# Kernel optimization log

Hardware: AMD Instinct MI355X
Metric: run time of the kernel (lower is better)

Reference implementation:

```python
import jax, jax.numpy as jnp
import numpy as np

N_NODES = 100000
N_EDGES = 500000
HIDDEN = 256


def setup_inputs() -> dict:
    key = jax.random.key(0)
    k_x, k_e, k_w1, k_b1, k_w2, k_b2 = jax.random.split(key, 6)
    x = jax.random.normal(k_x, (N_NODES, HIDDEN), dtype=jnp.float32)
    edge_label_index = jax.random.randint(k_e, (2, N_EDGES), 0, N_NODES, dtype=jnp.int64)
    # fc1: Linear(2*hidden -> hidden); fc2: Linear(hidden -> 1). PyTorch stores W as [out, in].
    bound1 = 1.0 / np.sqrt(2 * HIDDEN)
    W1 = jax.random.uniform(k_w1, (HIDDEN, 2 * HIDDEN), dtype=jnp.float32, minval=-bound1, maxval=bound1)
    b1 = jax.random.uniform(k_b1, (HIDDEN,), dtype=jnp.float32, minval=-bound1, maxval=bound1)
    bound2 = 1.0 / np.sqrt(HIDDEN)
    W2 = jax.random.uniform(k_w2, (1, HIDDEN), dtype=jnp.float32, minval=-bound2, maxval=bound2)
    b2 = jax.random.uniform(k_b2, (1,), dtype=jnp.float32, minval=-bound2, maxval=bound2)
    return {"x": x, "edge_label_index": edge_label_index, "W1": W1, "b1": b1, "W2": W2, "b2": b2}


def reference(x, edge_label_index, W1, b1, W2, b2):
    # Gather endpoint features: [E, H] each
    feat_src = x[edge_label_index[0]]
    feat_dst = x[edge_label_index[1]]
    h = jnp.concatenate([feat_src, feat_dst], axis=1)  # [E, 2H]
    h = jax.nn.relu(h @ W1.T + b1)                      # [E, H]
    out = jax.nn.sigmoid(h @ W2.T + b2)                 # [E, 1]
    return out.reshape(-1)
```

## Files before the change

### kernel.cpp

```cpp
#include <hip/hip_runtime.h>
#include <math.h>

#define NNODES 100000
#define MT     64
#define NTILES 1563
#define NODESP (NTILES * MT)
#define NEDGES 500000
#define HID    256
#define K2     512
#define GEMM_GRID 256

typedef _Float16 h8v __attribute__((ext_vector_type(8)));
typedef _Float16 h2v __attribute__((ext_vector_type(2)));
typedef __fp16   fp16x2 __attribute__((ext_vector_type(2)));
typedef __bf16   bf16x8 __attribute__((ext_vector_type(8)));
typedef float    f32x4  __attribute__((ext_vector_type(4)));

__device__ __forceinline__ unsigned short f2bf(float f) {
    unsigned int u = __float_as_uint(f);
    u += 0x7FFFu + ((u >> 16) & 1u);
    return (unsigned short)(u >> 16);
}
__device__ __forceinline__ void async16(void* lds, const void* g) {
    __builtin_amdgcn_global_load_lds((const __attribute__((address_space(1))) void*)g,
                                     (__attribute__((address_space(3))) void*)lds, 16, 0, 0);
}

__global__ void cvt_w1h(const float* __restrict__ W1, _Float16* __restrict__ Bsw) {
    int t = blockIdx.x * 256 + threadIdx.x;
    if (t >= 8 * 32 * 64) return;
    int lane = t & 63, nt = (t >> 6) & 31, kt = t >> 11;
    int j = nt * 16 + (lane & 15);
    int k = kt * 32 + ((lane >> 4) << 3);
    const float* src = W1 + (size_t)(j & 255) * K2 + ((j >> 8) << 8) + k;
    union { _Float16 s[8]; uint4 v; } u;
#pragma unroll
    for (int jj = 0; jj < 8; ++jj) u.s[jj] = (_Float16)src[jj];
    ((uint4*)Bsw)[t] = u.v;
}

__global__ void cvt_w2p(const float* __restrict__ W2, float* __restrict__ w2p) {
    int t = threadIdx.x;
    int i = (t >> 2) & 15, nt = t & 3;
    w2p[t] = W2[(t & ~63) | (nt * 16 + i)];
}

__global__ __launch_bounds__(512, 2) void node_gemm6(
    const float* __restrict__ x,
    const _Float16* __restrict__ Bsw,
    const float* __restrict__ b1,
    _Float16* __restrict__ UV)
{
    __shared__ __align__(16) float Afs[2][64 * 256];
    const int tid  = threadIdx.x;
    const int lane = tid & 63;
    const int wave = tid >> 6;

    const h8v* B8 = (const h8v*)Bsw;
    h8v barr[8][4];
#pragma unroll
    for (int ks = 0; ks < 8; ++ks)
#pragma unroll
        for (int nt = 0; nt < 4; ++nt)
            barr[ks][nt] = B8[((size_t)(ks * 32 + wave * 4 + nt)) * 64 + lane];

    float b1v[4];
#pragma unroll
    for (int nt = 0; nt < 4; ++nt) {
        int col = wave * 64 + nt * 16 + (lane & 15);
        b1v[nt] = (col < 256) ? b1[col] : 0.0f;
    }

    const int rlo = lane & 15;
    const int chi = (lane >> 4) << 1;

    auto issue = [&](int tile, int buf) {
        uint4* A4 = (uint4*)Afs[buf];
#pragma unroll
        for (int i = 0; i < 8; ++i) {
            int idx  = wave * 8 + i;
            int ks   = idx >> 3;
            int mt   = (idx >> 1) & 3;
            int half = idx & 1;
            int row  = tile * MT + mt * 16 + rlo;
            int rl   = row < NNODES ? row : 0;
            int c    = ks * 8 + chi + half;
            async16(&A4[idx * 64], x + (size_t)rl * 256 + c * 4);
        }
    };

    int tile = blockIdx.x;
    issue(tile, 0);
    __syncthreads();
    int buf = 0;

    while (true) {
        int next = tile + GEMM_GRID;
        bool has_next = next < NTILES;
        if (has_next) issue(next, buf ^ 1);

        f32x4 acc[4][4] = {};
        const float4* AF = (const float4*)Afs[buf];
#pragma unroll
        for (int ks = 0; ks < 8; ++ks) {
#pragma unroll
            for (int mt = 0; mt < 4; ++mt) {
                int idx = (ks * 4 + mt) * 2;
                float4 r0 = AF[idx * 64 + lane];
                float4 r1 = AF[(idx + 1) * 64 + lane];
                union { fp16x2 p[4]; h8v v; } af;
                af.p[0] = __builtin_amdgcn_cvt_pkrtz(r0.x, r0.y);
                af.p[1] = __builtin_amdgcn_cvt_pkrtz(r0.z, r0.w);
                af.p[2] = __builtin_amdgcn_cvt_pkrtz(r1.x, r1.y);
                af.p[3] = __builtin_amdgcn_cvt_pkrtz(r1.z, r1.w);
#pragma unroll
                for (int nt = 0; nt < 4; ++nt)
                    acc[mt][nt] = __builtin_amdgcn_mfma_f32_16x16x32_f16(
                        af.v, barr[ks][nt], acc[mt][nt], 0, 0, 0);
            }
        }

#pragma unroll
        for (int mt = 0; mt < 4; ++mt) {
#pragma unroll
            for (int r = 0; r < 4; ++r) {
                int row = tile * MT + mt * 16 + ((lane >> 4) << 2) + r;
                union { _Float16 h[4]; uint2 v; } pk;
#pragma unroll
                for (int nt = 0; nt < 4; ++nt)
                    pk.h[nt] = (_Float16)(acc[mt][nt][r] + b1v[nt]);
                *(uint2*)(UV + (size_t)row * 512 + wave * 64 + (lane & 15) * 4) = pk.v;
            }
        }

        if (!has_next) break;
        __syncthreads();
        buf ^= 1;
        tile = next;
    }
}

__global__ __launch_bounds__(256) void edge_out5(
    const _Float16* __restrict__ UV,
    const int* __restrict__ ei,
    const float* __restrict__ w2p,
    const float* __restrict__ b2,
    float* __restrict__ out)
{
    const int tid = threadIdx.x;
    const int q   = tid & 31;
    const int g   = tid >> 5;
    const long e  = ((long)blockIdx.x * 8 + g) * 8;
    if (e >= NEDGES) return;

    int4 s0 = *(const int4*)(ei + e);
    int4 s1 = *(const int4*)(ei + e + 4);
    int4 d0 = *(const int4*)(ei + NEDGES + e);
    int4 d1 = *(const int4*)(ei + NEDGES + e + 4);
    int is[8] = {s0.x, s0.y, s0.z, s0.w, s1.x, s1.y, s1.z, s1.w};
    int id[8] = {d0.x, d0.y, d0.z, d0.w, d1.x, d1.y, d1.z, d1.w};

    union U8 { uint4 v; h2v h[4]; };
    const _Float16* up = UV + q * 8;

    U8 uu[8], vv[8];
#pragma unroll
    for (int ed = 0; ed < 8; ++ed) {
        uu[ed].v = *(const uint4*)(up + (size_t)is[ed] * 512);
        vv[ed].v = *(const uint4*)(up + (size_t)id[ed] * 512 + 256);
    }

    h2v w2h[4];
    {
        const float4* pw = (const float4*)w2p + q * 2;
        float4 c = pw[0], d = pw[1];
        w2h[0] = h2v{(_Float16)c.x, (_Float16)c.y};
        w2h[1] = h2v{(_Float16)c.z, (_Float16)c.w};
        w2h[2] = h2v{(_Float16)d.x, (_Float16)d.y};
        w2h[3] = h2v{(_Float16)d.z, (_Float16)d.w};
    }

    const h2v zz = {(_Float16)0.0f, (_Float16)0.0f};
    float z[8];
#pragma unroll
    for (int ed = 0; ed < 8; ++ed) {
        float zt = 0.f;
#pragma unroll
        for (int p = 0; p < 4; ++p) {
            h2v h = uu[ed].h[p] + vv[ed].h[p];
            h = __builtin_elementwise_max(h, zz);
            zt = __builtin_amdgcn_fdot2(h, w2h[p], zt, false);
        }
        z[ed] = zt;
    }
#pragma unroll
    for (int m = 1; m < 32; m <<= 1) {
#pragma unroll
        for (int ed = 0; ed < 8; ++ed)
            z[ed] += __shfl_xor(z[ed], m, 32);
    }
    if (q < 8) {
        float zq = (q == 0) ? z[0] : (q == 1) ? z[1] : (q == 2) ? z[2] :
                   (q == 3) ? z[3] : (q == 4) ? z[4] : (q == 5) ? z[5] :
                   (q == 6) ? z[6] : z[7];
        out[e + q] = 1.0f / (1.0f + expf(-(zq + b2[0])));
    }
}

__global__ void cvt_w1_r1(const float* __restrict__ W1, unsigned short* __restrict__ Bsw) {
    int t = blockIdx.x * 256 + threadIdx.x;
    if (t >= 16 * 16 * 64) return;
    int lane = t & 63, nt = (t >> 6) & 15, kt = t >> 10;
    int n = nt * 16 + (lane & 15);
    int k = kt * 32 + ((lane >> 4) << 3);
    const float* src = W1 + (size_t)n * K2 + k;
    union { unsigned short s[8]; uint4 v; } u;
#pragma unroll
    for (int j = 0; j < 8; ++j) u.s[j] = f2bf(src[j]);
    ((uint4*)Bsw)[t] = u.v;
}

__global__ __launch_bounds__(256) void edge_mlp_fb(
    const float* __restrict__ xf, const int* __restrict__ ei,
    const unsigned short* __restrict__ Bsw, const float* __restrict__ b1,
    const float* __restrict__ W2, const float* __restrict__ b2,
    float* __restrict__ out)
{
    __shared__ __align__(16) unsigned short Asw[8 * 4 * 64 * 8];
    __shared__ float es[64];
    const int tid = threadIdx.x, lane = tid & 63, wave = tid >> 6;
    const int e0 = blockIdx.x * 64;
    if (tid < 64) es[tid] = 0.0f;
    f32x4 acc[4][4] = {};
    const bf16x8* A8 = (const bf16x8*)Asw;
    const bf16x8* B8 = (const bf16x8*)Bsw;
    for (int h = 0; h < 2; ++h) {
#pragma unroll
        for (int i = 0; i < 8; ++i) {
            int m = i * 8 + wave * 2 + (lane >> 5);
            int e = e0 + m;
            int ee = (e < NEDGES) ? e : 0;
            int node = ei[(size_t)h * NEDGES + ee];
            int chunk = lane & 31;
            const float4* p = (const float4*)(xf + ((size_t)node << 8) + (chunk << 3));
            float4 a = p[0], bq = p[1];
            union { unsigned short s[8]; uint4 v4; } u;
            u.s[0] = f2bf(a.x);  u.s[1] = f2bf(a.y);  u.s[2] = f2bf(a.z);  u.s[3] = f2bf(a.w);
            u.s[4] = f2bf(bq.x); u.s[5] = f2bf(bq.y); u.s[6] = f2bf(bq.z); u.s[7] = f2bf(bq.w);
            int ktl = chunk >> 2, qq = chunk & 3;
            int u16 = ((ktl * 4 + (m >> 4)) << 6) + (qq << 4) + (m & 15);
            u16 ^= (u16 >> 8) & 7;
            ((uint4*)Asw)[u16] = u.v4;
        }
        __syncthreads();
#pragma unroll
        for (int kt = 0; kt < 8; ++kt) {
            bf16x8 af[4], bfr[4];
#pragma unroll
            for (int mt = 0; mt < 4; ++mt) {
                int u16 = ((kt * 4 + mt) << 6) + lane;
                u16 ^= (u16 >> 8) & 7;
                af[mt] = A8[u16];
            }
#pragma unroll
            for (int nt = 0; nt < 4; ++nt)
                bfr[nt] = B8[(((h * 8 + kt) << 4) + (wave << 2) + nt) * 64 + lane];
#pragma unroll
            for (int mt = 0; mt < 4; ++mt)
#pragma unroll
                for (int nt = 0; nt < 4; ++nt)
                    acc[mt][nt] = __builtin_amdgcn_mfma_f32_16x16x32_bf16(
                        af[mt], bfr[nt], acc[mt][nt], 0, 0, 0);
        }
        __syncthreads();
    }
    float w2v[4], b1v[4];
#pragma unroll
    for (int nt = 0; nt < 4; ++nt) {
        int n = (wave << 6) + (nt << 4) + (lane & 15);
        w2v[nt] = W2[n]; b1v[nt] = b1[n];
    }
#pragma unroll
    for (int mt = 0; mt < 4; ++mt) {
#pragma unroll
        for (int r = 0; r < 4; ++r) {
            float p = 0.0f;
#pragma unroll
            for (int nt = 0; nt < 4; ++nt) {
                float hv = acc[mt][nt][r] + b1v[nt];
                p = fmaf(fmaxf(hv, 0.0f), w2v[nt], p);
            }
            p += __shfl_xor(p, 1, 16);
            p += __shfl_xor(p, 2, 16);
            p += __shfl_xor(p, 4, 16);
            p += __shfl_xor(p, 8, 16);
            if ((lane & 15) == 0)
                atomicAdd(&es[(mt << 4) + ((lane >> 4) << 2) + r], p);
        }
    }
    __syncthreads();
    if (tid < 64) {
        int e = e0 + tid;
        if (e < NEDGES) out[e] = 1.0f / (1.0f + expf(-(es[tid] + b2[0])));
    }
}

extern "C" void kernel_launch(void* const* d_in, const int* in_sizes, int n_in,
                              void* d_out, int out_size, void* d_ws, size_t ws_size,
                              hipStream_t stream) {
    const float* x  = (const float*)d_in[0];
    const int*   ei = (const int*)d_in[1];
    const float* W1 = (const float*)d_in[2];
    const float* b1 = (const float*)d_in[3];
    const float* W2 = (const float*)d_in[4];
    const float* b2 = (const float*)d_in[5];
    float* out = (float*)d_out;

    const size_t BSW_BYTES = 1 << 18;
    const size_t W2P_BYTES = 4096;
    const size_t UV_BYTES  = (size_t)NODESP * K2 * 2;
    const size_t NEED_A = BSW_BYTES + W2P_BYTES + UV_BYTES;

    if (ws_size >= NEED_A) {
        _Float16* Bsw = (_Float16*)d_ws;
        float*    w2p = (float*)((char*)d_ws + BSW_BYTES);
        _Float16* UV  = (_Float16*)((char*)d_ws + BSW_BYTES + W2P_BYTES);
        cvt_w1h<<<64, 256, 0, stream>>>(W1, Bsw);
        cvt_w2p<<<1, 256, 0, stream>>>(W2, w2p);
        node_gemm6<<<GEMM_GRID, 512, 0, stream>>>(x, Bsw, b1, UV);
        edge_out5<<<7813, 256, 0, stream>>>(UV, ei, w2p, b2, out);
    } else {
        unsigned short* Bsw = (unsigned short*)d_ws;
        cvt_w1_r1<<<64, 256, 0, stream>>>(W1, Bsw);
        edge_mlp_fb<<<(NEDGES + 63) / 64, 256, 0, stream>>>(x, ei, Bsw, b1, W2, b2, out);
    }
}
```

Before: 256.8 us.

## Load GEMM A operand directly from global into registers, dropping LDS staging

The node GEMM no longer stages x tiles in shared memory through async global-to-LDS copies with double buffering and barriers. Each wave now reads its own rows straight from global memory into registers, prefetching one MFMA step ahead. This removes the 128KB LDS footprint and the block-wide barriers, but every wave reloads the same A rows, so L2 traffic rises eightfold and the register-level prefetch hides less latency than the deeper LDS pipeline did.

```diff
diff --git a/kernel.cpp b/kernel.cpp
--- a/kernel.cpp
+++ b/kernel.cpp
@@ -21,10 +21,6 @@
     u += 0x7FFFu + ((u >> 16) & 1u);
     return (unsigned short)(u >> 16);
 }
-__device__ __forceinline__ void async16(void* lds, const void* g) {
-    __builtin_amdgcn_global_load_lds((const __attribute__((address_space(1))) void*)g,
-                                     (__attribute__((address_space(3))) void*)lds, 16, 0, 0);
-}
 
 __global__ void cvt_w1h(const float* __restrict__ W1, _Float16* __restrict__ Bsw) {
     int t = blockIdx.x * 256 + threadIdx.x;
@@ -45,13 +41,12 @@
     w2p[t] = W2[(t & ~63) | (nt * 16 + i)];
 }
 
-__global__ __launch_bounds__(512, 2) void node_gemm6(
+__global__ __launch_bounds__(512, 2) void node_gemm7(
     const float* __restrict__ x,
     const _Float16* __restrict__ Bsw,
     const float* __restrict__ b1,
     _Float16* __restrict__ UV)
 {
-    __shared__ __align__(16) float Afs[2][64 * 256];
     const int tid  = threadIdx.x;
     const int lane = tid & 63;
     const int wave = tid >> 6;
@@ -71,53 +66,42 @@
         b1v[nt] = (col < 256) ? b1[col] : 0.0f;
     }
 
-    const int rlo = lane & 15;
-    const int chi = (lane >> 4) << 1;
-
-    auto issue = [&](int tile, int buf) {
-        uint4* A4 = (uint4*)Afs[buf];
-#pragma unroll
-        for (int i = 0; i < 8; ++i) {
-            int idx  = wave * 8 + i;
-            int ks   = idx >> 3;
-            int mt   = (idx >> 1) & 3;
-            int half = idx & 1;
-            int row  = tile * MT + mt * 16 + rlo;
-            int rl   = row < NNODES ? row : 0;
-            int c    = ks * 8 + chi + half;
-            async16(&A4[idx * 64], x + (size_t)rl * 256 + c * 4);
-        }
-    };
-
-    int tile = blockIdx.x;
-    issue(tile, 0);
-    __syncthreads();
-    int buf = 0;
-
-    while (true) {
-        int next = tile + GEMM_GRID;
-        bool has_next = next < NTILES;
-        if (has_next) issue(next, buf ^ 1);
+    const int rlo   = lane & 15;
+    const int kbase = (lane >> 4) << 3;
+
+    for (int tile = blockIdx.x; tile < NTILES; tile += GEMM_GRID) {
+        const float* rp[4];
+#pragma unroll
+        for (int mt = 0; mt < 4; ++mt) {
+            int row = tile * MT + mt * 16 + rlo;
+            int rl  = row < NNODES ? row : 0;
+            rp[mt] = x + (size_t)rl * 256 + kbase;
+        }
 
         f32x4 acc[4][4] = {};
-        const float4* AF = (const float4*)Afs[buf];
-#pragma unroll
-        for (int ks = 0; ks < 8; ++ks) {
-#pragma unroll
-            for (int mt = 0; mt < 4; ++mt) {
-                int idx = (ks * 4 + mt) * 2;
-                float4 r0 = AF[idx * 64 + lane];
-                float4 r1 = AF[(idx + 1) * 64 + lane];
-                union { fp16x2 p[4]; h8v v; } af;
-                af.p[0] = __builtin_amdgcn_cvt_pkrtz(r0.x, r0.y);
-                af.p[1] = __builtin_amdgcn_cvt_pkrtz(r0.z, r0.w);
-                af.p[2] = __builtin_amdgcn_cvt_pkrtz(r1.x, r1.y);
-                af.p[3] = __builtin_amdgcn_cvt_pkrtz(r1.z, r1.w);
-#pragma unroll
-                for (int nt = 0; nt < 4; ++nt)
-                    acc[mt][nt] = __builtin_amdgcn_mfma_f32_16x16x32_f16(
-                        af.v, barr[ks][nt], acc[mt][nt], 0, 0, 0);
+        float4 c0 = ((const float4*)rp[0])[0];
+        float4 c1 = ((const float4*)rp[0])[1];
+#pragma unroll
+        for (int s = 0; s < 32; ++s) {
+            const int ks = s >> 2, mt = s & 3;
+            float4 n0, n1;
+            if (s < 31) {
+                const int ks2 = (s + 1) >> 2, mt2 = (s + 1) & 3;
+                const float4* p = (const float4*)(rp[mt2] + ks2 * 32);
+                n0 = p[0];
+                n1 = p[1];
             }
+            union { fp16x2 p4[4]; h8v v; } af;
+            af.p4[0] = __builtin_amdgcn_cvt_pkrtz(c0.x, c0.y);
+            af.p4[1] = __builtin_amdgcn_cvt_pkrtz(c0.z, c0.w);
+            af.p4[2] = __builtin_amdgcn_cvt_pkrtz(c1.x, c1.y);
+            af.p4[3] = __builtin_amdgcn_cvt_pkrtz(c1.z, c1.w);
+#pragma unroll
+            for (int nt = 0; nt < 4; ++nt)
+                acc[mt][nt] = __builtin_amdgcn_mfma_f32_16x16x32_f16(
+                    af.v, barr[ks][nt], acc[mt][nt], 0, 0, 0);
+            c0 = n0;
+            c1 = n1;
         }
 
 #pragma unroll
@@ -132,11 +116,6 @@
                 *(uint2*)(UV + (size_t)row * 512 + wave * 64 + (lane & 15) * 4) = pk.v;
             }
         }
-
-        if (!has_next) break;
-        __syncthreads();
-        buf ^= 1;
-        tile = next;
     }
 }
 
@@ -327,7 +306,7 @@
         _Float16* UV  = (_Float16*)((char*)d_ws + BSW_BYTES + W2P_BYTES);
         cvt_w1h<<<64, 256, 0, stream>>>(W1, Bsw);
         cvt_w2p<<<1, 256, 0, stream>>>(W2, w2p);
-        node_gemm6<<<GEMM_GRID, 512, 0, stream>>>(x, Bsw, b1, UV);
+        node_gemm7<<<GEMM_GRID, 512, 0, stream>>>(x, Bsw, b1, UV);
         edge_out5<<<7813, 256, 0, stream>>>(UV, ei, w2p, b2, out);
     } else {
         unsigned short* Bsw = (unsigned short*)d_ws;
```

Result: slower. 337.3 us (+31.3%).
